# Optimization experiments

Hardware: AMD Instinct MI355X
Metric: run time of the kernel (lower is better)

The kernel has to match this reference:

```python
import jax, jax.numpy as jnp
import numpy as np

NUM_RELATIONS = 8
NUM_BASES = 4
IN_CH, HID, OUT_CH = 128, 64, 64
N_NODES, N_EDGES = 50000, 500000


def rgcn_conv(x, edge_src, edge_dst, edge_type, basis, comp, root, bias):
    """PyG RGCNConv with basis decomposition and per-relation mean aggregation.
    basis: [B, in, out], comp: [R, B], root: [in, out], bias: [out].
    W_r = sum_b comp[r, b] * basis[b]; msg_e = x[src_e] @ W_{type_e};
    aggregate mean over incoming edges per (node, relation), sum over relations,
    then add root transform and bias.
    """
    n = x.shape[0]
    out_dim = basis.shape[2]
    # Project once through all bases: [N, B, out]  (cheap: B=4)
    h = jnp.einsum('ni,bio->nbo', x, basis)
    # Per-edge message: contract gathered basis features with per-edge comp coeffs
    msg = jnp.einsum('eb,ebo->eo', comp[edge_type], h[edge_src])  # [E, out]
    # Mean aggregation per (dst, relation): segment id = dst*R + relation
    seg = edge_dst * NUM_RELATIONS + edge_type
    sums = jax.ops.segment_sum(msg, seg, num_segments=n * NUM_RELATIONS)
    cnt = jax.ops.segment_sum(jnp.ones((msg.shape[0], 1), msg.dtype), seg,
                              num_segments=n * NUM_RELATIONS)
    mean = sums / jnp.maximum(cnt, 1.0)
    agg = mean.reshape(n, NUM_RELATIONS, out_dim).sum(axis=1)
    return agg + x @ root + bias


def setup_inputs() -> dict:
    key = jax.random.key(0)
    ks = jax.random.split(key, 12)
    s1 = 1.0 / np.sqrt(IN_CH)
    s2 = 1.0 / np.sqrt(HID)
    return {
        'x': jax.random.normal(ks[0], (N_NODES, IN_CH), jnp.float32),
        'edge_index': jax.random.randint(ks[1], (2, N_EDGES), 0, N_NODES, jnp.int64),
        'edge_type': jax.random.randint(ks[2], (N_EDGES,), 0, NUM_RELATIONS, jnp.int64),
        'basis1': jax.random.normal(ks[3], (NUM_BASES, IN_CH, HID), jnp.float32) * s1,
        'comp1': jax.random.normal(ks[4], (NUM_RELATIONS, NUM_BASES), jnp.float32) * 0.5,
        'root1': jax.random.normal(ks[5], (IN_CH, HID), jnp.float32) * s1,
        'bias1': jnp.zeros((HID,), jnp.float32),
        'basis2': jax.random.normal(ks[6], (NUM_BASES, HID, OUT_CH), jnp.float32) * s2,
        'comp2': jax.random.normal(ks[7], (NUM_RELATIONS, NUM_BASES), jnp.float32) * 0.5,
        'root2': jax.random.normal(ks[8], (HID, OUT_CH), jnp.float32) * s2,
        'bias2': jnp.zeros((OUT_CH,), jnp.float32),
    }


def reference(x, edge_index, edge_type, basis1, comp1, root1, bias1,
              basis2, comp2, root2, bias2):
    src, dst = edge_index[0], edge_index[1]
    h = rgcn_conv(x, src, dst, edge_type, basis1, comp1, root1, bias1)
    h = jax.nn.relu(h)
    out = rgcn_conv(h, src, dst, edge_type, basis2, comp2, root2, bias2)
    return out
```

## Files before the change

kernel.cpp:

```cpp
#include <hip/hip_runtime.h>
#include <cstddef>

#define NREL 8
#define SCAN_TILE 4096

typedef __bf16 bf16x8 __attribute__((ext_vector_type(8)));
typedef float f32x4 __attribute__((ext_vector_type(4)));

__device__ __forceinline__ unsigned f2bf_u(float f) {
    unsigned u = __float_as_uint(f);
    u += 0x7FFFu + ((u >> 16) & 1u);
    return u >> 16;
}
__device__ __forceinline__ short f2bf(float f) { return (short)f2bf_u(f); }
__device__ __forceinline__ int pack2bf(float lo, float hi) {
    return (int)(f2bf_u(lo) | (f2bf_u(hi) << 16));
}
__device__ __forceinline__ float bfval(unsigned short g) {
    return __uint_as_float((unsigned)g << 16);
}

__global__ __launch_bounds__(256) void zero_kernel(int4* __restrict__ p, int n16)
{
    int i = blockIdx.x * 256 + threadIdx.x;
    if (i < n16) p[i] = make_int4(0, 0, 0, 0);
}

__global__ __launch_bounds__(256) void hist_kernel(const int* __restrict__ dst,
                                                   const int* __restrict__ et,
                                                   int* __restrict__ cnt8, int E)
{
    int e = blockIdx.x * 256 + threadIdx.x;
    if (e < E) atomicAdd(&cnt8[dst[e] * NREL + et[e]], 1);
}

__global__ __launch_bounds__(256) void scan_part(const int* __restrict__ cnt8,
                                                 int* __restrict__ tsum, int n)
{
    int base = blockIdx.x * SCAN_TILE;
    int s = 0;
    for (int i = threadIdx.x; i < SCAN_TILE; i += 256) {
        int idx = base + i;
        if (idx < n) {
            int4 a = ((const int4*)cnt8)[idx * 2];
            int4 b = ((const int4*)cnt8)[idx * 2 + 1];
            s += a.x + a.y + a.z + a.w + b.x + b.y + b.z + b.w;
        }
    }
    for (int d = 1; d < 64; d <<= 1) s += __shfl_xor(s, d, 64);
    __shared__ int ws[4];
    if ((threadIdx.x & 63) == 0) ws[threadIdx.x >> 6] = s;
    __syncthreads();
    if (threadIdx.x == 0) tsum[blockIdx.x] = ws[0] + ws[1] + ws[2] + ws[3];
}

__global__ void scan_mid(int* __restrict__ tsum, int* __restrict__ offs_n, int nt)
{
    if (threadIdx.x == 0) {
        int run = 0;
        for (int i = 0; i < nt; ++i) { int t = tsum[i]; tsum[i] = run; run += t; }
        *offs_n = run;
    }
}

__global__ __launch_bounds__(256) void scan_final(const int* __restrict__ cnt8,
                                                  const int* __restrict__ tsum,
                                                  int* __restrict__ offs, int n)
{
    const int lane = threadIdx.x & 63, wid = threadIdx.x >> 6;
    int base = blockIdx.x * SCAN_TILE + threadIdx.x * 16;
    int v[16]; int s = 0;
#pragma unroll
    for (int j = 0; j < 16; ++j) {
        int idx = base + j;
        int dv = 0;
        if (idx < n) {
            int4 a = ((const int4*)cnt8)[idx * 2];
            int4 b = ((const int4*)cnt8)[idx * 2 + 1];
            dv = a.x + a.y + a.z + a.w + b.x + b.y + b.z + b.w;
        }
        v[j] = dv; s += dv;
    }
    int inc = s;
    for (int d = 1; d < 64; d <<= 1) {
        int t = __shfl_up(inc, d, 64);
        if (lane >= d) inc += t;
    }
    __shared__ int wsum[4];
    if (lane == 63) wsum[wid] = inc;
    __syncthreads();
    int run = tsum[blockIdx.x] + (inc - s);
    for (int k = 0; k < wid; ++k) run += wsum[k];
#pragma unroll
    for (int j = 0; j < 16; ++j) {
        int idx = base + j;
        if (idx < n) offs[idx] = run;
        run += v[j];
    }
}

__global__ __launch_bounds__(256) void scatter_kernel(const int* __restrict__ src,
                                                      const int* __restrict__ dst,
                                                      const int* __restrict__ et,
                                                      const int* __restrict__ offs,
                                                      int* __restrict__ cursor,
                                                      const int* __restrict__ cnt8,
                                                      int2* __restrict__ edgeP, int E)
{
    int e = blockIdx.x * 256 + threadIdx.x;
    if (e >= E) return;
    int d = dst[e], r = et[e], s = src[e];
    int c = cnt8[d * NREL + r];
    float inv = 1.0f / (float)(c > 1 ? c : 1);
    int pos = offs[d] + atomicAdd(&cursor[d], 1);
    edgeP[pos] = make_int2(s * NREL + r, __float_as_int(inv));
}

template<int K>
__global__ __launch_bounds__(256) void wfrag_kernel(const float* __restrict__ basis,
                                                    const float* __restrict__ root,
                                                    const float* __restrict__ comp,
                                                    short* __restrict__ Wf)
{
    constexpr int NK = K / 32;
    int tid = blockIdx.x * 256 + threadIdx.x;
    if (tid >= 36 * NK * 64) return;
    int lane = tid & 63, slot = tid >> 6;
    int ks = slot % NK, t = slot / NK;
    int kg = lane >> 4, lr = lane & 15;
    int k0 = ks * 32 + kg * 8;
    union { short s[8]; int4 v; } u;
#pragma unroll
    for (int e = 0; e < 8; ++e) {
        int k = k0 + e;
        float v;
        if (t < 32) {
            int rr = t >> 2, ch = (t & 3) * 16 + lr;
            v = comp[rr * 4 + 0] * basis[((size_t)0 * K + k) * 64 + ch]
              + comp[rr * 4 + 1] * basis[((size_t)1 * K + k) * 64 + ch]
              + comp[rr * 4 + 2] * basis[((size_t)2 * K + k) * 64 + ch]
              + comp[rr * 4 + 3] * basis[((size_t)3 * K + k) * 64 + ch];
        } else {
            v = root[(size_t)k * 64 + (t - 32) * 16 + lr];
        }
        u.s[e] = f2bf(v);
    }
    *(int4*)(Wf + (size_t)tid * 8) = u.v;
}

template<int K>
__global__ __launch_bounds__(256) void afrag_kernel(const float* __restrict__ x,
                                                    short* __restrict__ xf,
                                                    int N, int NT)
{
    constexpr int NK = K / 32;
    int tid = blockIdx.x * 256 + threadIdx.x;
    if (tid >= NT * NK * 64) return;
    int lane = tid & 63, slot = tid >> 6;
    int ks = slot % NK, rt = slot / NK;
    int kg = lane >> 4, lr = lane & 15;
    int row = rt * 16 + lr, k = ks * 32 + kg * 8;
    union { short s[8]; int4 v; } u;
    if (row < N) {
        const float* xp = x + (size_t)row * K + k;
        float4 a = *(const float4*)xp;
        float4 b = *(const float4*)(xp + 4);
        u.s[0] = f2bf(a.x); u.s[1] = f2bf(a.y); u.s[2] = f2bf(a.z); u.s[3] = f2bf(a.w);
        u.s[4] = f2bf(b.x); u.s[5] = f2bf(b.y); u.s[6] = f2bf(b.z); u.s[7] = f2bf(b.w);
    } else {
        u.v = make_int4(0, 0, 0, 0);
    }
    *(int4*)(xf + (size_t)tid * 8) = u.v;
}

template<int K>
__global__ __launch_bounds__(256) void gemm_mfma(const short* __restrict__ xf,
                                                 const short* __restrict__ Wf,
                                                 const float* __restrict__ bias,
                                                 short* __restrict__ hr,
                                                 float* __restrict__ yinit, int N)
{
    constexpr int NK = K / 32;
    __shared__ short lds[12 * NK * 512];

    const int w = threadIdx.x >> 6, lane = threadIdx.x & 63;
    const int kg = lane >> 4, lr = lane & 15;
    const int rt = blockIdx.x * 4 + w;
    const int g0 = blockIdx.y * 3;

    {
        const int4* gsrc = (const int4*)(Wf + (size_t)g0 * 4 * NK * 512);
        int4* ldst = (int4*)lds;
#pragma unroll
        for (int i = threadIdx.x; i < 12 * NK * 64; i += 256)
            ldst[i] = gsrc[i];
    }

    bf16x8 afrag[NK];
    const short* ap = xf + ((size_t)rt * NK * 64 + lane) * 8;
#pragma unroll
    for (int ks = 0; ks < NK; ++ks)
        afrag[ks] = *(const bf16x8*)(ap + ks * 512);

    f32x4 acc[12];
#pragma unroll
    for (int t = 0; t < 12; ++t) acc[t] = (f32x4){0.f, 0.f, 0.f, 0.f};

    __syncthreads();

#pragma unroll
    for (int tt = 0; tt < 12; ++tt) {
#pragma unroll
        for (int ks = 0; ks < NK; ++ks) {
            bf16x8 bfrag = *(const bf16x8*)(lds + (tt * NK + ks) * 512 + lane * 8);
            acc[tt] = __builtin_amdgcn_mfma_f32_16x16x32_bf16(afrag[ks], bfrag,
                                                              acc[tt], 0, 0, 0);
        }
    }

    float b0 = bias[lr], b1 = bias[16 + lr], b2 = bias[32 + lr], b3 = bias[48 + lr];

    const int drow0 = rt * 16 + kg * 4;
#pragma unroll
    for (int r = 0; r < 4; ++r) {
        int dr = drow0 + r;
        if (dr >= N) break;
#pragma unroll
        for (int gg = 0; gg < 3; ++gg) {
            int g = g0 + gg;
            if (g < 8) {
                int u0 = pack2bf(acc[gg * 4 + 0][r], acc[gg * 4 + 1][r]);
                int u1 = pack2bf(acc[gg * 4 + 2][r], acc[gg * 4 + 3][r]);
                *(int2*)(hr + (size_t)dr * 512 + g * 64 + lr * 4) = make_int2(u0, u1);
            } else {
                float4 o = make_float4(acc[gg * 4 + 0][r] + b0, acc[gg * 4 + 1][r] + b1,
                                       acc[gg * 4 + 2][r] + b2, acc[gg * 4 + 3][r] + b3);
                *(float4*)(yinit + (size_t)dr * 64 + lr * 4) = o;
            }
        }
    }
}

template<bool BF16OUT>
__global__ __launch_bounds__(256) void agg_kernel(const int* __restrict__ offs,
                                                  const int2* __restrict__ edgeP,
                                                  const short* __restrict__ hr,
                                                  const float* __restrict__ init,
                                                  float* __restrict__ outF,
                                                  short* __restrict__ outB, int N)
{
    const int dst = blockIdx.x * 4 + (threadIdx.x >> 6);
    const int l = threadIdx.x & 63;
    if (dst >= N) return;

    const unsigned short* hp = (const unsigned short*)hr;
    float acc = init[(size_t)dst * 64 + l];
    int e0 = offs[dst], e1 = offs[dst + 1];

    int e = e0;
    for (; e + 3 < e1; e += 4) {
        int2 p0 = edgeP[e],     p1 = edgeP[e + 1];
        int2 p2 = edgeP[e + 2], p3 = edgeP[e + 3];
        unsigned short g0 = hp[(size_t)p0.x * 64 + l];
        unsigned short g1 = hp[(size_t)p1.x * 64 + l];
        unsigned short g2 = hp[(size_t)p2.x * 64 + l];
        unsigned short g3 = hp[(size_t)p3.x * 64 + l];
        acc = fmaf(bfval(g0), __int_as_float(p0.y), acc);
        acc = fmaf(bfval(g1), __int_as_float(p1.y), acc);
        acc = fmaf(bfval(g2), __int_as_float(p2.y), acc);
        acc = fmaf(bfval(g3), __int_as_float(p3.y), acc);
    }
    for (; e < e1; ++e) {
        int2 p0 = edgeP[e];
        unsigned short g0 = hp[(size_t)p0.x * 64 + l];
        acc = fmaf(bfval(g0), __int_as_float(p0.y), acc);
    }

    int tc = (l & 3) * 16 + (l >> 2);
    if (BF16OUT) {
        int rt2 = dst >> 4, lr2 = dst & 15;
        int ks2 = tc >> 5, kg2 = (tc >> 3) & 3, e2 = tc & 7;
        outB[(((size_t)rt2 * 2 + ks2) * 64 + kg2 * 16 + lr2) * 8 + e2] =
            f2bf(fmaxf(acc, 0.f));
    } else {
        outF[(size_t)dst * 64 + tc] = acc;
    }
}

extern "C" void kernel_launch(void* const* d_in, const int* in_sizes, int n_in,
                              void* d_out, int out_size, void* d_ws, size_t ws_size,
                              hipStream_t stream)
{
    const float* x      = (const float*)d_in[0];
    const int*   ei     = (const int*)d_in[1];
    const int*   et     = (const int*)d_in[2];
    const float* basis1 = (const float*)d_in[3];
    const float* comp1  = (const float*)d_in[4];
    const float* root1  = (const float*)d_in[5];
    const float* bias1  = (const float*)d_in[6];
    const float* basis2 = (const float*)d_in[7];
    const float* comp2  = (const float*)d_in[8];
    const float* root2  = (const float*)d_in[9];
    const float* bias2  = (const float*)d_in[10];
    float* out = (float*)d_out;

    const int N = in_sizes[0] / 128;
    const int E = in_sizes[2];
    const int* src  = ei;
    const int* dstp = ei + E;

    const int gblk = (N + 63) / 64;
    const int NT   = gblk * 4;
    const int ablk = (N + 3) / 4;

    char* p = (char*)d_ws;
    auto carve = [&](size_t bytes) -> char* {
        char* q = p; p += (bytes + 255) & ~(size_t)255; return q;
    };
    int*   cursor  = (int*)carve((size_t)N * 4);
    int*   cnt8    = (int*)carve((size_t)N * NREL * 4);
    char*  zend    = p;
    int*   offs    = (int*)carve((size_t)(N + 1) * 4);
    int*   tsum    = (int*)carve(256 * 4);
    int2*  edgeP   = (int2*)carve((size_t)E * 8);
    short* Wf1     = (short*)carve((size_t)36 * 4 * 64 * 8 * 2);
    short* Wf2     = (short*)carve((size_t)36 * 2 * 64 * 8 * 2);
    float* yinit   = (float*)carve((size_t)N * 64 * 4);
    short* xf1     = (short*)carve((size_t)NT * 4 * 64 * 8 * 2);
    short* xf2     = (short*)carve((size_t)NT * 2 * 64 * 8 * 2);
    short* hr      = (short*)carve((size_t)N * 512 * 2);

    const int zn16 = (int)((zend - (char*)cursor) / 16);
    const int ntiles = (N + SCAN_TILE - 1) / SCAN_TILE;

    zero_kernel<<<(zn16 + 255) / 256, 256, 0, stream>>>((int4*)cursor, zn16);
    wfrag_kernel<128><<<(36 * 4 * 64 + 255) / 256, 256, 0, stream>>>(basis1, root1, comp1, Wf1);
    wfrag_kernel<64><<<(36 * 2 * 64 + 255) / 256, 256, 0, stream>>>(basis2, root2, comp2, Wf2);
    afrag_kernel<128><<<(NT * 4 * 64 + 255) / 256, 256, 0, stream>>>(x, xf1, N, NT);
    gemm_mfma<128><<<dim3(gblk, 3), 256, 0, stream>>>(xf1, Wf1, bias1, hr, yinit, N);

    hist_kernel<<<(E + 255) / 256, 256, 0, stream>>>(dstp, et, cnt8, E);
    scan_part<<<ntiles, 256, 0, stream>>>(cnt8, tsum, N);
    scan_mid<<<1, 64, 0, stream>>>(tsum, offs + N, ntiles);
    scan_final<<<ntiles, 256, 0, stream>>>(cnt8, tsum, offs, N);
    scatter_kernel<<<(E + 255) / 256, 256, 0, stream>>>(src, dstp, et, offs, cursor,
                                                        cnt8, edgeP, E);

    agg_kernel<true><<<ablk, 256, 0, stream>>>(offs, edgeP, hr, yinit, nullptr, xf2, N);

    gemm_mfma<64><<<dim3(gblk, 3), 256, 0, stream>>>(xf2, Wf2, bias2, hr, yinit, N);
    agg_kernel<false><<<ablk, 256, 0, stream>>>(offs, edgeP, hr, yinit, out, nullptr, N);
}
```

Baseline: 192.8 us.

## Fuse prep kernels, drop scan_mid, and make GEMM grid-stride persistent

Merges the zeroing, both weight-fragment builds and the input-fragment conversion into one prep kernel. It removes the single-thread scan_mid launch by having each scan_final block sum the preceding tile totals itself, and writes offs[N]=E directly. The GEMM becomes grid-stride over a fixed 196x3 grid, so each block loads its weight tiles into LDS once and reuses them across several row tiles. The first GEMM is moved after the CSR build. The aim is fewer launches and fewer redundant LDS weight loads, at the cost of less parallelism per GEMM launch.

```diff
diff --git a/kernel.cpp b/kernel.cpp
--- a/kernel.cpp
+++ b/kernel.cpp
@@ -20,111 +20,13 @@
     return __uint_as_float((unsigned)g << 16);
 }
 
-__global__ __launch_bounds__(256) void zero_kernel(int4* __restrict__ p, int n16)
-{
-    int i = blockIdx.x * 256 + threadIdx.x;
-    if (i < n16) p[i] = make_int4(0, 0, 0, 0);
-}
-
-__global__ __launch_bounds__(256) void hist_kernel(const int* __restrict__ dst,
-                                                   const int* __restrict__ et,
-                                                   int* __restrict__ cnt8, int E)
-{
-    int e = blockIdx.x * 256 + threadIdx.x;
-    if (e < E) atomicAdd(&cnt8[dst[e] * NREL + et[e]], 1);
-}
-
-__global__ __launch_bounds__(256) void scan_part(const int* __restrict__ cnt8,
-                                                 int* __restrict__ tsum, int n)
-{
-    int base = blockIdx.x * SCAN_TILE;
-    int s = 0;
-    for (int i = threadIdx.x; i < SCAN_TILE; i += 256) {
-        int idx = base + i;
-        if (idx < n) {
-            int4 a = ((const int4*)cnt8)[idx * 2];
-            int4 b = ((const int4*)cnt8)[idx * 2 + 1];
-            s += a.x + a.y + a.z + a.w + b.x + b.y + b.z + b.w;
-        }
-    }
-    for (int d = 1; d < 64; d <<= 1) s += __shfl_xor(s, d, 64);
-    __shared__ int ws[4];
-    if ((threadIdx.x & 63) == 0) ws[threadIdx.x >> 6] = s;
-    __syncthreads();
-    if (threadIdx.x == 0) tsum[blockIdx.x] = ws[0] + ws[1] + ws[2] + ws[3];
-}
-
-__global__ void scan_mid(int* __restrict__ tsum, int* __restrict__ offs_n, int nt)
-{
-    if (threadIdx.x == 0) {
-        int run = 0;
-        for (int i = 0; i < nt; ++i) { int t = tsum[i]; tsum[i] = run; run += t; }
-        *offs_n = run;
-    }
-}
-
-__global__ __launch_bounds__(256) void scan_final(const int* __restrict__ cnt8,
-                                                  const int* __restrict__ tsum,
-                                                  int* __restrict__ offs, int n)
-{
-    const int lane = threadIdx.x & 63, wid = threadIdx.x >> 6;
-    int base = blockIdx.x * SCAN_TILE + threadIdx.x * 16;
-    int v[16]; int s = 0;
-#pragma unroll
-    for (int j = 0; j < 16; ++j) {
-        int idx = base + j;
-        int dv = 0;
-        if (idx < n) {
-            int4 a = ((const int4*)cnt8)[idx * 2];
-            int4 b = ((const int4*)cnt8)[idx * 2 + 1];
-            dv = a.x + a.y + a.z + a.w + b.x + b.y + b.z + b.w;
-        }
-        v[j] = dv; s += dv;
-    }
-    int inc = s;
-    for (int d = 1; d < 64; d <<= 1) {
-        int t = __shfl_up(inc, d, 64);
-        if (lane >= d) inc += t;
-    }
-    __shared__ int wsum[4];
-    if (lane == 63) wsum[wid] = inc;
-    __syncthreads();
-    int run = tsum[blockIdx.x] + (inc - s);
-    for (int k = 0; k < wid; ++k) run += wsum[k];
-#pragma unroll
-    for (int j = 0; j < 16; ++j) {
-        int idx = base + j;
-        if (idx < n) offs[idx] = run;
-        run += v[j];
-    }
-}
-
-__global__ __launch_bounds__(256) void scatter_kernel(const int* __restrict__ src,
-                                                      const int* __restrict__ dst,
-                                                      const int* __restrict__ et,
-                                                      const int* __restrict__ offs,
-                                                      int* __restrict__ cursor,
-                                                      const int* __restrict__ cnt8,
-                                                      int2* __restrict__ edgeP, int E)
-{
-    int e = blockIdx.x * 256 + threadIdx.x;
-    if (e >= E) return;
-    int d = dst[e], r = et[e], s = src[e];
-    int c = cnt8[d * NREL + r];
-    float inv = 1.0f / (float)(c > 1 ? c : 1);
-    int pos = offs[d] + atomicAdd(&cursor[d], 1);
-    edgeP[pos] = make_int2(s * NREL + r, __float_as_int(inv));
-}
-
 template<int K>
-__global__ __launch_bounds__(256) void wfrag_kernel(const float* __restrict__ basis,
-                                                    const float* __restrict__ root,
-                                                    const float* __restrict__ comp,
-                                                    short* __restrict__ Wf)
+__device__ __forceinline__ void wfrag_body(const float* __restrict__ basis,
+                                           const float* __restrict__ root,
+                                           const float* __restrict__ comp,
+                                           short* __restrict__ Wf, int tid)
 {
     constexpr int NK = K / 32;
-    int tid = blockIdx.x * 256 + threadIdx.x;
-    if (tid >= 36 * NK * 64) return;
     int lane = tid & 63, slot = tid >> 6;
     int ks = slot % NK, t = slot / NK;
     int kg = lane >> 4, lr = lane & 15;
@@ -148,21 +50,16 @@
     *(int4*)(Wf + (size_t)tid * 8) = u.v;
 }
 
-template<int K>
-__global__ __launch_bounds__(256) void afrag_kernel(const float* __restrict__ x,
-                                                    short* __restrict__ xf,
-                                                    int N, int NT)
-{
-    constexpr int NK = K / 32;
-    int tid = blockIdx.x * 256 + threadIdx.x;
-    if (tid >= NT * NK * 64) return;
+__device__ __forceinline__ void afrag_body128(const float* __restrict__ x,
+                                              short* __restrict__ xf, int N, int tid)
+{
     int lane = tid & 63, slot = tid >> 6;
-    int ks = slot % NK, rt = slot / NK;
+    int ks = slot & 3, rt = slot >> 2;
     int kg = lane >> 4, lr = lane & 15;
     int row = rt * 16 + lr, k = ks * 32 + kg * 8;
     union { short s[8]; int4 v; } u;
     if (row < N) {
-        const float* xp = x + (size_t)row * K + k;
+        const float* xp = x + (size_t)row * 128 + k;
         float4 a = *(const float4*)xp;
         float4 b = *(const float4*)(xp + 4);
         u.s[0] = f2bf(a.x); u.s[1] = f2bf(a.y); u.s[2] = f2bf(a.z); u.s[3] = f2bf(a.w);
@@ -173,69 +70,181 @@
     *(int4*)(xf + (size_t)tid * 8) = u.v;
 }
 
+__global__ __launch_bounds__(256) void prep_kernel(
+    const float* __restrict__ basis1, const float* __restrict__ root1,
+    const float* __restrict__ comp1,  const float* __restrict__ basis2,
+    const float* __restrict__ root2,  const float* __restrict__ comp2,
+    const float* __restrict__ x,
+    short* __restrict__ Wf1, short* __restrict__ Wf2, short* __restrict__ xf1,
+    int4* __restrict__ zp, int zn16, int* __restrict__ offsN,
+    int E, int N, int NT)
+{
+    int b = blockIdx.x;
+    const int zb = (zn16 + 255) >> 8;
+    if (b < zb) {
+        int i = b * 256 + threadIdx.x;
+        if (i < zn16) zp[i] = make_int4(0, 0, 0, 0);
+        if (b == 0 && threadIdx.x == 0) *offsN = E;
+        return;
+    }
+    b -= zb;
+    if (b < 36) { wfrag_body<128>(basis1, root1, comp1, Wf1, b * 256 + threadIdx.x); return; }
+    b -= 36;
+    if (b < 18) { wfrag_body<64>(basis2, root2, comp2, Wf2, b * 256 + threadIdx.x); return; }
+    b -= 18;
+    int tid = b * 256 + threadIdx.x;
+    if (tid < NT * 256) afrag_body128(x, xf1, N, tid);
+}
+
+__global__ __launch_bounds__(256) void hist_kernel(const int* __restrict__ dst,
+                                                   const int* __restrict__ et,
+                                                   int* __restrict__ cnt8, int E)
+{
+    int e = blockIdx.x * 256 + threadIdx.x;
+    if (e < E) atomicAdd(&cnt8[dst[e] * NREL + et[e]], 1);
+}
+
+__global__ __launch_bounds__(256) void scan_part(const int* __restrict__ cnt8,
+                                                 int* __restrict__ tsum, int n)
+{
+    int base = blockIdx.x * SCAN_TILE;
+    int s = 0;
+    for (int i = threadIdx.x; i < SCAN_TILE; i += 256) {
+        int idx = base + i;
+        if (idx < n) {
+            int4 a = ((const int4*)cnt8)[idx * 2];
+            int4 b = ((const int4*)cnt8)[idx * 2 + 1];
+            s += a.x + a.y + a.z + a.w + b.x + b.y + b.z + b.w;
+        }
+    }
+    for (int d = 1; d < 64; d <<= 1) s += __shfl_xor(s, d, 64);
+    __shared__ int ws[4];
+    if ((threadIdx.x & 63) == 0) ws[threadIdx.x >> 6] = s;
+    __syncthreads();
+    if (threadIdx.x == 0) tsum[blockIdx.x] = ws[0] + ws[1] + ws[2] + ws[3];
+}
+
+__global__ __launch_bounds__(256) void scan_final(const int* __restrict__ cnt8,
+                                                  const int* __restrict__ tsum,
+                                                  int* __restrict__ offs, int n)
+{
+    const int lane = threadIdx.x & 63, wid = threadIdx.x >> 6;
+    int tbase = 0;
+    for (int i = 0; i < blockIdx.x; ++i) tbase += tsum[i];
+    int base = blockIdx.x * SCAN_TILE + threadIdx.x * 16;
+    int v[16]; int s = 0;
+#pragma unroll
+    for (int j = 0; j < 16; ++j) {
+        int idx = base + j;
+        int dv = 0;
+        if (idx < n) {
+            int4 a = ((const int4*)cnt8)[idx * 2];
+            int4 b = ((const int4*)cnt8)[idx * 2 + 1];
+            dv = a.x + a.y + a.z + a.w + b.x + b.y + b.z + b.w;
+        }
+        v[j] = dv; s += dv;
+    }
+    int inc = s;
+    for (int d = 1; d < 64; d <<= 1) {
+        int t = __shfl_up(inc, d, 64);
+        if (lane >= d) inc += t;
+    }
+    __shared__ int wsum[4];
+    if (lane == 63) wsum[wid] = inc;
+    __syncthreads();
+    int run = tbase + (inc - s);
+    for (int k = 0; k < wid; ++k) run += wsum[k];
+#pragma unroll
+    for (int j = 0; j < 16; ++j) {
+        int idx = base + j;
+        if (idx < n) offs[idx] = run;
+        run += v[j];
+    }
+}
+
+__global__ __launch_bounds__(256) void scatter_kernel(const int* __restrict__ src,
+                                                      const int* __restrict__ dst,
+                                                      const int* __restrict__ et,
+                                                      const int* __restrict__ offs,
+                                                      int* __restrict__ cursor,
+                                                      const int* __restrict__ cnt8,
+                                                      int2* __restrict__ edgeP, int E)
+{
+    int e = blockIdx.x * 256 + threadIdx.x;
+    if (e >= E) return;
+    int d = dst[e], r = et[e], s = src[e];
+    int c = cnt8[d * NREL + r];
+    float inv = 1.0f / (float)(c > 1 ? c : 1);
+    int pos = offs[d] + atomicAdd(&cursor[d], 1);
+    edgeP[pos] = make_int2(s * NREL + r, __float_as_int(inv));
+}
+
 template<int K>
 __global__ __launch_bounds__(256) void gemm_mfma(const short* __restrict__ xf,
                                                  const short* __restrict__ Wf,
                                                  const float* __restrict__ bias,
                                                  short* __restrict__ hr,
-                                                 float* __restrict__ yinit, int N)
+                                                 float* __restrict__ yinit,
+                                                 int N, int gblk)
 {
     constexpr int NK = K / 32;
     __shared__ short lds[12 * NK * 512];
 
     const int w = threadIdx.x >> 6, lane = threadIdx.x & 63;
     const int kg = lane >> 4, lr = lane & 15;
-    const int rt = blockIdx.x * 4 + w;
     const int g0 = blockIdx.y * 3;
 
     {
         const int4* gsrc = (const int4*)(Wf + (size_t)g0 * 4 * NK * 512);
         int4* ldst = (int4*)lds;
-#pragma unroll
         for (int i = threadIdx.x; i < 12 * NK * 64; i += 256)
             ldst[i] = gsrc[i];
     }
 
-    bf16x8 afrag[NK];
-    const short* ap = xf + ((size_t)rt * NK * 64 + lane) * 8;
-#pragma unroll
-    for (int ks = 0; ks < NK; ++ks)
-        afrag[ks] = *(const bf16x8*)(ap + ks * 512);
-
-    f32x4 acc[12];
-#pragma unroll
-    for (int t = 0; t < 12; ++t) acc[t] = (f32x4){0.f, 0.f, 0.f, 0.f};
+    float b0 = bias[lr], b1 = bias[16 + lr], b2 = bias[32 + lr], b3 = bias[48 + lr];
 
     __syncthreads();
 
-#pragma unroll
-    for (int tt = 0; tt < 12; ++tt) {
-#pragma unroll
-        for (int ks = 0; ks < NK; ++ks) {
-            bf16x8 bfrag = *(const bf16x8*)(lds + (tt * NK + ks) * 512 + lane * 8);
-            acc[tt] = __builtin_amdgcn_mfma_f32_16x16x32_bf16(afrag[ks], bfrag,
-                                                              acc[tt], 0, 0, 0);
-        }
-    }
-
-    float b0 = bias[lr], b1 = bias[16 + lr], b2 = bias[32 + lr], b3 = bias[48 + lr];
-
-    const int drow0 = rt * 16 + kg * 4;
-#pragma unroll
-    for (int r = 0; r < 4; ++r) {
-        int dr = drow0 + r;
-        if (dr >= N) break;
-#pragma unroll
-        for (int gg = 0; gg < 3; ++gg) {
-            int g = g0 + gg;
-            if (g < 8) {
-                int u0 = pack2bf(acc[gg * 4 + 0][r], acc[gg * 4 + 1][r]);
-                int u1 = pack2bf(acc[gg * 4 + 2][r], acc[gg * 4 + 3][r]);
-                *(int2*)(hr + (size_t)dr * 512 + g * 64 + lr * 4) = make_int2(u0, u1);
-            } else {
-                float4 o = make_float4(acc[gg * 4 + 0][r] + b0, acc[gg * 4 + 1][r] + b1,
-                                       acc[gg * 4 + 2][r] + b2, acc[gg * 4 + 3][r] + b3);
-                *(float4*)(yinit + (size_t)dr * 64 + lr * 4) = o;
+    for (int bx = blockIdx.x; bx < gblk; bx += gridDim.x) {
+        const int rt = bx * 4 + w;
+
+        bf16x8 afrag[NK];
+        const short* ap = xf + ((size_t)rt * NK * 64 + lane) * 8;
+#pragma unroll
+        for (int ks = 0; ks < NK; ++ks)
+            afrag[ks] = *(const bf16x8*)(ap + ks * 512);
+
+        f32x4 acc[12];
+#pragma unroll
+        for (int t = 0; t < 12; ++t) acc[t] = (f32x4){0.f, 0.f, 0.f, 0.f};
+
+#pragma unroll
+        for (int tt = 0; tt < 12; ++tt) {
+#pragma unroll
+            for (int ks = 0; ks < NK; ++ks) {
+                bf16x8 bfrag = *(const bf16x8*)(lds + (tt * NK + ks) * 512 + lane * 8);
+                acc[tt] = __builtin_amdgcn_mfma_f32_16x16x32_bf16(afrag[ks], bfrag,
+                                                                  acc[tt], 0, 0, 0);
+            }
+        }
+
+        const int drow0 = rt * 16 + kg * 4;
+#pragma unroll
+        for (int r = 0; r < 4; ++r) {
+            int dr = drow0 + r;
+            if (dr >= N) break;
+#pragma unroll
+            for (int gg = 0; gg < 3; ++gg) {
+                int g = g0 + gg;
+                if (g < 8) {
+                    int u0 = pack2bf(acc[gg * 4 + 0][r], acc[gg * 4 + 1][r]);
+                    int u1 = pack2bf(acc[gg * 4 + 2][r], acc[gg * 4 + 3][r]);
+                    *(int2*)(hr + (size_t)dr * 512 + g * 64 + lr * 4) = make_int2(u0, u1);
+                } else {
+                    float4 o = make_float4(acc[gg * 4 + 0][r] + b0, acc[gg * 4 + 1][r] + b1,
+                                           acc[gg * 4 + 2][r] + b2, acc[gg * 4 + 3][r] + b3);
+                    *(float4*)(yinit + (size_t)dr * 64 + lr * 4) = o;
+                }
             }
         }
     }
@@ -331,23 +340,22 @@
     short* hr      = (short*)carve((size_t)N * 512 * 2);
 
     const int zn16 = (int)((zend - (char*)cursor) / 16);
+    const int zb   = (zn16 + 255) / 256;
     const int ntiles = (N + SCAN_TILE - 1) / SCAN_TILE;
 
-    zero_kernel<<<(zn16 + 255) / 256, 256, 0, stream>>>((int4*)cursor, zn16);
-    wfrag_kernel<128><<<(36 * 4 * 64 + 255) / 256, 256, 0, stream>>>(basis1, root1, comp1, Wf1);
-    wfrag_kernel<64><<<(36 * 2 * 64 + 255) / 256, 256, 0, stream>>>(basis2, root2, comp2, Wf2);
-    afrag_kernel<128><<<(NT * 4 * 64 + 255) / 256, 256, 0, stream>>>(x, xf1, N, NT);
-    gemm_mfma<128><<<dim3(gblk, 3), 256, 0, stream>>>(xf1, Wf1, bias1, hr, yinit, N);
+    prep_kernel<<<zb + 36 + 18 + NT, 256, 0, stream>>>(
+        basis1, root1, comp1, basis2, root2, comp2, x,
+        Wf1, Wf2, xf1, (int4*)cursor, zn16, offs + N, E, N, NT);
 
     hist_kernel<<<(E + 255) / 256, 256, 0, stream>>>(dstp, et, cnt8, E);
     scan_part<<<ntiles, 256, 0, stream>>>(cnt8, tsum, N);
-    scan_mid<<<1, 64, 0, stream>>>(tsum, offs + N, ntiles);
     scan_final<<<ntiles, 256, 0, stream>>>(cnt8, tsum, offs, N);
     scatter_kernel<<<(E + 255) / 256, 256, 0, stream>>>(src, dstp, et, offs, cursor,
                                                         cnt8, edgeP, E);
 
+    gemm_mfma<128><<<dim3(196, 3), 256, 0, stream>>>(xf1, Wf1, bias1, hr, yinit, N, gblk);
     agg_kernel<true><<<ablk, 256, 0, stream>>>(offs, edgeP, hr, yinit, nullptr, xf2, N);
 
-    gemm_mfma<64><<<dim3(gblk, 3), 256, 0, stream>>>(xf2, Wf2, bias2, hr, yinit, N);
+    gemm_mfma<64><<<dim3(196, 3), 256, 0, stream>>>(xf2, Wf2, bias2, hr, yinit, N, gblk);
     agg_kernel<false><<<ablk, 256, 0, stream>>>(offs, edgeP, hr, yinit, out, nullptr, N);
 }
```

After: 189.8 us. Within noise of the previous version (-1.5%).
